# Optimization experiments

Hardware: AMD Instinct MI355X
Metric: run time of the kernel (lower is better)

The kernel has to match this reference:

```python
import jax, jax.numpy as jnp
import numpy as np

DIM = 1024
DIM_HEAD = 64
HEADS = 16
NUM_LATENTS = 64
INNER = DIM_HEAD * HEADS  # 1024


def setup_inputs() -> dict:
    key = jax.random.key(0)
    ks = jax.random.split(key, 6)
    b, m, n = 8, 4, 1024
    x = jax.random.normal(ks[0], (b, m, n, DIM), dtype=jnp.float32)
    latents = jax.random.normal(ks[1], (NUM_LATENTS, DIM), dtype=jnp.float32)
    # Linear weights stored as (in, out); no bias for q/kv, bias for out (matches nn.Linear defaults)
    Wq = jax.random.normal(ks[2], (DIM, INNER), dtype=jnp.float32) * (DIM ** -0.5)
    Wkv = jax.random.normal(ks[3], (DIM, INNER * 2), dtype=jnp.float32) * (DIM ** -0.5)
    Wout = jax.random.normal(ks[4], (INNER, DIM), dtype=jnp.float32) * (INNER ** -0.5)
    bout = jax.random.normal(ks[5], (DIM,), dtype=jnp.float32) * 0.01
    return {"x": x, "latents": latents, "Wq": Wq, "Wkv": Wkv, "Wout": Wout, "bout": bout}


def reference(x, latents, Wq, Wkv, Wout, bout):
    b, m, n, d = x.shape
    h, dh = HEADS, DIM_HEAD
    scale = dh ** -0.5

    # q from latents: [n_lat, inner] -> [h, i, dh]
    q = (latents @ Wq).reshape(NUM_LATENTS, h, dh).transpose(1, 0, 2) * scale

    # k, v from media tokens: [b, m, n, 2*inner] -> two [b, h, m, n, dh]
    kv = x @ Wkv
    k, v = jnp.split(kv, 2, axis=-1)
    k = k.reshape(b, m, n, h, dh).transpose(0, 3, 1, 2, 4)  # b h m n dh
    v = v.reshape(b, m, n, h, dh).transpose(0, 3, 1, 2, 4)

    # latent k, v: [n_lat, 2*inner] -> [h, n_lat, dh] broadcast to [b, h, m, n_lat, dh]
    lkv = latents @ Wkv
    lk, lv = jnp.split(lkv, 2, axis=-1)
    lk = jnp.broadcast_to(lk.reshape(NUM_LATENTS, h, dh).transpose(1, 0, 2)[None, :, None], (b, h, m, NUM_LATENTS, dh))
    lv = jnp.broadcast_to(lv.reshape(NUM_LATENTS, h, dh).transpose(1, 0, 2)[None, :, None], (b, h, m, NUM_LATENTS, dh))

    k = jnp.concatenate((k, lk), axis=-2)  # b h m (n + n_lat) dh
    v = jnp.concatenate((v, lv), axis=-2)

    sim = jnp.einsum('hid,bhmjd->bhmij', q, k)
    attn = jax.nn.softmax(sim, axis=-1)  # stable softmax (max-subtract internal)
    out = jnp.einsum('bhmij,bhmjd->bhmid', attn, v)  # b h m i dh
    out = out.transpose(0, 2, 3, 1, 4).reshape(b, m, NUM_LATENTS, h * dh)  # b m i inner
    return out @ Wout + bout
```

## Files before the change

kernel.cpp:

```cpp
#include <hip/hip_runtime.h>
#include <cstdint>

typedef __attribute__((ext_vector_type(8))) __bf16 bf16x8;
typedef __attribute__((ext_vector_type(4))) float f32x4;
typedef __attribute__((ext_vector_type(8))) unsigned short u16x8;
typedef __attribute__((ext_vector_type(4))) unsigned short u16x4;

__device__ __forceinline__ unsigned short f2bf(float f) {
    union { float f; unsigned u; } v; v.f = f;
    unsigned u = v.u;
    return (unsigned short)((u + 0x7FFFu + ((u >> 16) & 1u)) >> 16);
}

__device__ __forceinline__ void gload_lds16(const void* g, void* l) {
    auto gp = reinterpret_cast<__attribute__((address_space(1))) unsigned*>(
        reinterpret_cast<uintptr_t>(g));
    auto lp = reinterpret_cast<__attribute__((address_space(3))) unsigned*>(
        reinterpret_cast<uintptr_t>(l));
    __builtin_amdgcn_global_load_lds(gp, lp, 16, 0, 0);
}

__global__ __launch_bounds__(256) void cvt_kernel(const float* __restrict__ in,
                                                  unsigned short* __restrict__ out, int n4) {
    int idx = blockIdx.x * 256 + threadIdx.x;
    int stride = gridDim.x * 256;
    for (int i = idx; i < n4; i += stride) {
        float4 v = ((const float4*)in)[i];
        u16x4 o;
        o.x = f2bf(v.x); o.y = f2bf(v.y); o.z = f2bf(v.z); o.w = f2bf(v.w);
        ((u16x4*)out)[i] = o;
    }
}

__global__ __launch_bounds__(256) void transpose_cvt(const float* __restrict__ in,
                                                     unsigned short* __restrict__ out,
                                                     int R, int C) {
    __shared__ float t[32][33];
    int c0 = blockIdx.x * 32, r0 = blockIdx.y * 32;
    int tx = threadIdx.x, ty = threadIdx.y;
    for (int i = ty; i < 32; i += 8)
        t[i][tx] = in[(size_t)(r0 + i) * C + c0 + tx];
    __syncthreads();
    for (int i = ty; i < 32; i += 8)
        out[(size_t)(c0 + i) * R + r0 + tx] = f2bf(t[tx][i]);
}

__global__ __launch_bounds__(256) void gemm128p(const unsigned short* __restrict__ A,
                                                const unsigned short* __restrict__ Bt,
                                                void* __restrict__ C,
                                                const float* __restrict__ bias,
                                                unsigned short* __restrict__ vT,
                                                int M, int N, int K, float scale, int split,
                                                int c_f32, int vstart) {
    __shared__ unsigned short lds[3][2][4096];
    int ntx = N >> 7;
    int nwg = gridDim.x, bid = blockIdx.x, swz = bid;
    if ((nwg & 7) == 0) { int cpx = nwg >> 3; swz = (bid & 7) * cpx + (bid >> 3); }
    int m0 = (swz / ntx) << 7, n0 = (swz % ntx) << 7;
    int tid = threadIdx.x, lane = tid & 63, w = tid >> 6;
    int wm = w >> 1, wn = w & 1;
    int lr = lane & 15, lg = lane >> 4;
    int gq = lg ^ ((lr >> 1) & 3);
    int nkt = K >> 5;

    int arow = tid >> 2;
    int sgl = (tid & 3) ^ ((arow >> 1) & 3);
    int ra0 = m0 + arow;      if (ra0 > M - 1) ra0 = M - 1;
    int ra1 = m0 + 64 + arow; if (ra1 > M - 1) ra1 = M - 1;
    const unsigned short* a0 = A + (size_t)ra0 * K + (sgl << 3);
    const unsigned short* a1 = A + (size_t)ra1 * K + (sgl << 3);
    const unsigned short* b0 = Bt + (size_t)(n0 + arow) * K + (sgl << 3);
    const unsigned short* b1 = Bt + (size_t)(n0 + 64 + arow) * K + (sgl << 3);

    f32x4 acc[4][4] = {};

#define ST_A128(bi, kt) do { \
        gload_lds16(a0 + ((kt) << 5), &lds[bi][0][w << 9]); \
        gload_lds16(a1 + ((kt) << 5), &lds[bi][0][2048 + (w << 9)]); } while (0)
#define ST_B128(bi, kt) do { \
        gload_lds16(b0 + ((kt) << 5), &lds[bi][1][w << 9]); \
        gload_lds16(b1 + ((kt) << 5), &lds[bi][1][2048 + (w << 9)]); } while (0)

    ST_A128(0, 0); ST_B128(0, 0);
    ST_A128(1, 1); ST_B128(1, 1);

    int buf = 0;
    for (int t = 0; t < nkt; ++t) {
        asm volatile("s_waitcnt vmcnt(4) lgkmcnt(0)" ::: "memory");
        __builtin_amdgcn_sched_barrier(0);
        __builtin_amdgcn_s_barrier();
        __builtin_amdgcn_sched_barrier(0);
        int st = t + 2; if (st >= nkt) st = nkt - 1;
        int sbuf = buf + 2; if (sbuf >= 3) sbuf -= 3;
        ST_A128(sbuf, st);
        ST_B128(sbuf, st);
        const unsigned short* pa = &lds[buf][0][((wm << 6) + lr) * 32 + (gq << 3)];
        const unsigned short* pb = &lds[buf][1][((wn << 6) + lr) * 32 + (gq << 3)];
        bf16x8 af[4], bfr[4];
#pragma unroll
        for (int nt = 0; nt < 4; nt++) bfr[nt] = *(const bf16x8*)(pb + nt * 512);
#pragma unroll
        for (int mt = 0; mt < 4; mt++) af[mt] = *(const bf16x8*)(pa + mt * 512);
        __builtin_amdgcn_s_setprio(1);
#pragma unroll
        for (int mt = 0; mt < 4; mt++)
#pragma unroll
            for (int nt = 0; nt < 4; nt++)
                acc[mt][nt] = __builtin_amdgcn_mfma_f32_16x16x32_bf16(af[mt], bfr[nt], acc[mt][nt], 0, 0, 0);
        __builtin_amdgcn_s_setprio(0);
        buf++; if (buf == 3) buf = 0;
    }
#undef ST_A128
#undef ST_B128

#pragma unroll
    for (int mt = 0; mt < 4; mt++) {
#pragma unroll
        for (int nt = 0; nt < 4; nt++) {
            int col = n0 + (wn << 6) + (nt << 4) + lr;
            float sc = (col < split) ? scale : 1.0f;
            float bv = bias ? bias[col] : 0.0f;
#pragma unroll
            for (int r = 0; r < 4; r++) {
                int row = m0 + (wm << 6) + (mt << 4) + (lg << 2) + r;
                if (row < M) {
                    float v = acc[mt][nt][r] * sc + bv;
                    if (vT && col >= vstart) vT[(size_t)(col - vstart) * 64 + row] = f2bf(v);
                    else if (c_f32) ((float*)C)[(size_t)row * N + col] = v;
                    else ((unsigned short*)C)[(size_t)row * N + col] = f2bf(v);
                }
            }
        }
    }
}

__global__ __launch_bounds__(512, 2) void gemm256(const unsigned short* __restrict__ A,
                                                  const unsigned short* __restrict__ Bt,
                                                  unsigned short* __restrict__ kb,
                                                  unsigned short* __restrict__ vbT,
                                                  int M, int N, int K) {
    __shared__ unsigned short lds[2][32768];
    int nkt = K >> 6;
    int ntx = N >> 8;
    int nwg = gridDim.x, bid = blockIdx.x, swz = bid;
    if ((nwg & 7) == 0) { int cpx = nwg >> 3; swz = (bid & 7) * cpx + (bid >> 3); }
    int m0 = (swz / ntx) << 8, n0 = (swz % ntx) << 8;
    int tid = threadIdx.x, lane = tid & 63, w = tid >> 6;
    int wm = w >> 2, wn = w & 3;
    int lr = lane & 15, lg = lane >> 4;

    int srow = lane >> 3;
    int sg = (lane & 7) ^ srow;
    const unsigned short* aS = A + (size_t)(m0 + (w << 3) + srow) * K + (sg << 3);
    const unsigned short* bS = Bt + (size_t)(n0 + (w << 3) + srow) * K + (sg << 3);
    size_t rs64 = (size_t)64 * K;

    int baseA = (wm << 13) + lr * 64;
    int baseB = 16384 + (wn << 12) + lr * 64;
    int kg0 = (((0 << 2) + lg) ^ (lr & 7)) << 3;
    int kg1 = (((1 << 2) + lg) ^ (lr & 7)) << 3;

    f32x4 acc[8][4] = {};

#define ST_A(bi, kt) do { \
        gload_lds16(aS + ((size_t)(kt) << 6),          &lds[bi][(w << 9)]); \
        gload_lds16(aS + rs64 + ((size_t)(kt) << 6),   &lds[bi][4096 + (w << 9)]); \
        gload_lds16(aS + 2*rs64 + ((size_t)(kt) << 6), &lds[bi][8192 + (w << 9)]); \
        gload_lds16(aS + 3*rs64 + ((size_t)(kt) << 6), &lds[bi][12288 + (w << 9)]); } while (0)
#define ST_B(bi, kt) do { \
        gload_lds16(bS + ((size_t)(kt) << 6),          &lds[bi][16384 + (w << 9)]); \
        gload_lds16(bS + rs64 + ((size_t)(kt) << 6),   &lds[bi][20480 + (w << 9)]); \
        gload_lds16(bS + 2*rs64 + ((size_t)(kt) << 6), &lds[bi][24576 + (w << 9)]); \
        gload_lds16(bS + 3*rs64 + ((size_t)(kt) << 6), &lds[bi][28672 + (w << 9)]); } while (0)

    ST_A(0, 0);
    ST_B(0, 0);

    for (int t = 0; t < nkt; ++t) {
        int cur = t & 1, nxt = cur ^ 1;
        int st = t + 1; if (st >= nkt) st = nkt - 1;
        const unsigned short* L = &lds[cur][0];
        bf16x8 af[4], bfr[4];

        ST_A(nxt, st);
        __builtin_amdgcn_sched_barrier(0);
        asm volatile("s_waitcnt vmcnt(4)" ::: "memory");
        __builtin_amdgcn_sched_barrier(0);
        __builtin_amdgcn_s_barrier();
        __builtin_amdgcn_sched_barrier(0);
#pragma unroll
        for (int nt = 0; nt < 4; nt++) bfr[nt] = *(const bf16x8*)(L + baseB + nt * 1024 + kg0);
#pragma unroll
        for (int i = 0; i < 4; i++) af[i] = *(const bf16x8*)(L + baseA + i * 1024 + kg0);
        asm volatile("s_waitcnt lgkmcnt(0)" ::: "memory");
        __builtin_amdgcn_sched_barrier(0);
        __builtin_amdgcn_s_setprio(1);
#pragma unroll
        for (int i = 0; i < 4; i++)
#pragma unroll
            for (int nt = 0; nt < 4; nt++)
                acc[i][nt] = __builtin_amdgcn_mfma_f32_16x16x32_bf16(af[i], bfr[nt], acc[i][nt], 0, 0, 0);
        __builtin_amdgcn_s_setprio(0);

        ST_B(nxt, st);
#pragma unroll
        for (int i = 0; i < 4; i++) af[i] = *(const bf16x8*)(L + baseA + (i + 4) * 1024 + kg0);
        asm volatile("s_waitcnt lgkmcnt(0)" ::: "memory");
        __builtin_amdgcn_sched_barrier(0);
        __builtin_amdgcn_s_setprio(1);
#pragma unroll
        for (int i = 0; i < 4; i++)
#pragma unroll
            for (int nt = 0; nt < 4; nt++)
                acc[i + 4][nt] = __builtin_amdgcn_mfma_f32_16x16x32_bf16(af[i], bfr[nt], acc[i + 4][nt], 0, 0, 0);
        __builtin_amdgcn_s_setprio(0);

#pragma unroll
        for (int nt = 0; nt < 4; nt++) bfr[nt] = *(const bf16x8*)(L + baseB + nt * 1024 + kg1);
#pragma unroll
        for (int i = 0; i < 4; i++) af[i] = *(const bf16x8*)(L + baseA + i * 1024 + kg1);
        asm volatile("s_waitcnt lgkmcnt(0)" ::: "memory");
        __builtin_amdgcn_sched_barrier(0);
        __builtin_amdgcn_s_setprio(1);
#pragma unroll
        for (int i = 0; i < 4; i++)
#pragma unroll
            for (int nt = 0; nt < 4; nt++)
                acc[i][nt] = __builtin_amdgcn_mfma_f32_16x16x32_bf16(af[i], bfr[nt], acc[i][nt], 0, 0, 0);
        __builtin_amdgcn_s_setprio(0);

#pragma unroll
        for (int i = 0; i < 4; i++) af[i] = *(const bf16x8*)(L + baseA + (i + 4) * 1024 + kg1);
        asm volatile("s_waitcnt lgkmcnt(0)" ::: "memory");
        __builtin_amdgcn_sched_barrier(0);
        __builtin_amdgcn_s_barrier();
        __builtin_amdgcn_sched_barrier(0);
        __builtin_amdgcn_s_setprio(1);
#pragma unroll
        for (int i = 0; i < 4; i++)
#pragma unroll
            for (int nt = 0; nt < 4; nt++)
                acc[i + 4][nt] = __builtin_amdgcn_mfma_f32_16x16x32_bf16(af[i], bfr[nt], acc[i + 4][nt], 0, 0, 0);
        __builtin_amdgcn_s_setprio(0);
    }
#undef ST_A
#undef ST_B

    if (n0 < 1024) {
#pragma unroll
        for (int mt = 0; mt < 8; mt++) {
#pragma unroll
            for (int nt = 0; nt < 4; nt++) {
                int col = n0 + (wn << 6) + (nt << 4) + lr;
                size_t rbase = (size_t)(m0 + (wm << 7) + (mt << 4) + (lg << 2));
#pragma unroll
                for (int r = 0; r < 4; r++)
                    kb[(rbase + r) * 1024 + col] = f2bf(acc[mt][nt][r]);
            }
        }
    } else {
#pragma unroll
        for (int mt = 0; mt < 8; mt++) {
#pragma unroll
            for (int nt = 0; nt < 4; nt++) {
                int dg = n0 - 1024 + (wn << 6) + (nt << 4) + lr;
                int rbase = m0 + (wm << 7) + (mt << 4) + (lg << 2);
                int bm = rbase >> 10, j = rbase & 1023;
                u16x4 o;
                o.x = f2bf(acc[mt][nt][0]); o.y = f2bf(acc[mt][nt][1]);
                o.z = f2bf(acc[mt][nt][2]); o.w = f2bf(acc[mt][nt][3]);
                *(u16x4*)(&vbT[((size_t)(bm << 10) + dg) * 1024 + j]) = o;
            }
        }
    }
}

__global__ __launch_bounds__(256) void attn_kernel(const unsigned short* __restrict__ qg, int qstride,
                                                   const unsigned short* __restrict__ kb,
                                                   const unsigned short* __restrict__ vbT,
                                                   const unsigned short* __restrict__ lkg, int lstride,
                                                   const unsigned short* __restrict__ lvT,
                                                   unsigned short* __restrict__ og) {
    __shared__ unsigned short K_lds[64 * 72];
    __shared__ unsigned short V_lds[64 * 72];
    __shared__ unsigned short P_lds[4][16 * 72];
    int bm = blockIdx.x >> 4, h = blockIdx.x & 15;
    int tid = threadIdx.x, lane = tid & 63, w = tid >> 6;
    int lr = lane & 15, lg = lane >> 4;

    bf16x8 qf[2];
#pragma unroll
    for (int kk = 0; kk < 2; kk++)
        qf[kk] = *(const bf16x8*)(qg + (size_t)((w << 4) + lr) * qstride + (h << 6) + (kk << 5) + (lg << 3));

    f32x4 acc[4] = {};
    float m_run[4], l_run[4];
#pragma unroll
    for (int r = 0; r < 4; r++) { m_run[r] = -1e30f; l_run[r] = 0.0f; }

    int jrow = tid >> 2;
    int seg = (tid & 3) << 4;

    const unsigned short* k_s = kb + (size_t)((bm << 10) + jrow) * 1024 + (h << 6) + seg;
    const unsigned short* v_s = vbT + (size_t)((bm << 10) + (h << 6) + jrow) * 1024 + seg;
    u16x8 k0 = *(const u16x8*)(k_s);
    u16x8 k1 = *(const u16x8*)(k_s + 8);
    u16x8 v0 = *(const u16x8*)(v_s);
    u16x8 v1 = *(const u16x8*)(v_s + 8);

    for (int t = 0; t < 17; t++) {
        *(u16x8*)(&K_lds[jrow * 72 + seg]) = k0;
        *(u16x8*)(&K_lds[jrow * 72 + seg + 8]) = k1;
        *(u16x8*)(&V_lds[jrow * 72 + seg]) = v0;
        *(u16x8*)(&V_lds[jrow * 72 + seg + 8]) = v1;
        __syncthreads();

        u16x8 nk0 = k0, nk1 = k1, nv0 = v0, nv1 = v1;
        if (t < 16) {
            if (t < 15) {
                const unsigned short* ks = kb + (size_t)((bm << 10) + ((t + 1) << 6) + jrow) * 1024 + (h << 6) + seg;
                const unsigned short* vs = vbT + (size_t)((bm << 10) + (h << 6) + jrow) * 1024 + ((t + 1) << 6) + seg;
                nk0 = *(const u16x8*)(ks);
                nk1 = *(const u16x8*)(ks + 8);
                nv0 = *(const u16x8*)(vs);
                nv1 = *(const u16x8*)(vs + 8);
            } else {
                const unsigned short* ks = lkg + (size_t)jrow * lstride + (h << 6) + seg;
                const unsigned short* vs = lvT + (size_t)((h << 6) + jrow) * 64 + seg;
                nk0 = *(const u16x8*)(ks);
                nk1 = *(const u16x8*)(ks + 8);
                nv0 = *(const u16x8*)(vs);
                nv1 = *(const u16x8*)(vs + 8);
            }
        }

        f32x4 s[4] = {};
#pragma unroll
        for (int jt = 0; jt < 4; jt++) {
#pragma unroll
            for (int kk = 0; kk < 2; kk++) {
                bf16x8 kf = *(const bf16x8*)(&K_lds[(size_t)((jt << 4) + lr) * 72 + (kk << 5) + (lg << 3)]);
                s[jt] = __builtin_amdgcn_mfma_f32_16x16x32_bf16(qf[kk], kf, s[jt], 0, 0, 0);
            }
        }
#pragma unroll
        for (int r = 0; r < 4; r++) {
            float mx = fmaxf(fmaxf(s[0][r], s[1][r]), fmaxf(s[2][r], s[3][r]));
            mx = fmaxf(mx, __shfl_xor(mx, 1));
            mx = fmaxf(mx, __shfl_xor(mx, 2));
            mx = fmaxf(mx, __shfl_xor(mx, 4));
            mx = fmaxf(mx, __shfl_xor(mx, 8));
            float nm = fmaxf(m_run[r], mx);
            float fct = __expf(m_run[r] - nm);
            m_run[r] = nm;
            float p0 = __expf(s[0][r] - nm);
            float p1 = __expf(s[1][r] - nm);
            float p2 = __expf(s[2][r] - nm);
            float p3 = __expf(s[3][r] - nm);
            float sum = p0 + p1 + p2 + p3;
            sum += __shfl_xor(sum, 1);
            sum += __shfl_xor(sum, 2);
            sum += __shfl_xor(sum, 4);
            sum += __shfl_xor(sum, 8);
            l_run[r] = l_run[r] * fct + sum;
#pragma unroll
            for (int dt = 0; dt < 4; dt++) acc[dt][r] *= fct;
            int prow = ((lg << 2) + r) * 72;
            P_lds[w][prow + lr]      = f2bf(p0);
            P_lds[w][prow + 16 + lr] = f2bf(p1);
            P_lds[w][prow + 32 + lr] = f2bf(p2);
            P_lds[w][prow + 48 + lr] = f2bf(p3);
        }
#pragma unroll
        for (int jkk = 0; jkk < 2; jkk++) {
            bf16x8 pf = *(const bf16x8*)(&P_lds[w][(size_t)lr * 72 + (jkk << 5) + (lg << 3)]);
#pragma unroll
            for (int dt = 0; dt < 4; dt++) {
                bf16x8 vf = *(const bf16x8*)(&V_lds[(size_t)((dt << 4) + lr) * 72 + (jkk << 5) + (lg << 3)]);
                acc[dt] = __builtin_amdgcn_mfma_f32_16x16x32_bf16(pf, vf, acc[dt], 0, 0, 0);
            }
        }
        __syncthreads();
        k0 = nk0; k1 = nk1; v0 = nv0; v1 = nv1;
    }
#pragma unroll
    for (int dt = 0; dt < 4; dt++) {
#pragma unroll
        for (int r = 0; r < 4; r++) {
            int i = (w << 4) + (lg << 2) + r;
            float v = acc[dt][r] / l_run[r];
            og[(size_t)((bm << 6) + i) * 1024 + (h << 6) + (dt << 4) + lr] = f2bf(v);
        }
    }
}

extern "C" void kernel_launch(void* const* d_in, const int* in_sizes, int n_in,
                              void* d_out, int out_size, void* d_ws, size_t ws_size,
                              hipStream_t stream) {
    const float* x       = (const float*)d_in[0];
    const float* latents = (const float*)d_in[1];
    const float* Wq      = (const float*)d_in[2];
    const float* Wkv     = (const float*)d_in[3];
    const float* Wout    = (const float*)d_in[4];
    const float* bout    = (const float*)d_in[5];
    char* ws = (char*)d_ws;
    unsigned short* xb    = (unsigned short*)(ws);
    unsigned short* kb    = (unsigned short*)(ws + 67108864);
    unsigned short* vbT   = (unsigned short*)(ws + 134217728);
    unsigned short* wqkvt = (unsigned short*)(ws + 201326592);
    unsigned short* wkvt  = wqkvt + 1024 * 1024;
    unsigned short* woutt = (unsigned short*)(ws + 207618048);
    unsigned short* latb  = (unsigned short*)(ws + 209715200);
    unsigned short* qlkvb = (unsigned short*)(ws + 209846272);
    unsigned short* attnb = (unsigned short*)(ws + 210239488);
    unsigned short* lvT   = (unsigned short*)(ws + 214433792);

    cvt_kernel<<<2048, 256, 0, stream>>>(x, xb, 33554432 / 4);
    cvt_kernel<<<64, 256, 0, stream>>>(latents, latb, 65536 / 4);
    dim3 tb(32, 8);
    transpose_cvt<<<dim3(32, 32), tb, 0, stream>>>(Wq, wqkvt, 1024, 1024);
    transpose_cvt<<<dim3(64, 32), tb, 0, stream>>>(Wkv, wkvt, 1024, 2048);
    transpose_cvt<<<dim3(32, 32), tb, 0, stream>>>(Wout, woutt, 1024, 1024);
    gemm128p<<<24, 256, 0, stream>>>(latb, wqkvt, qlkvb, nullptr, lvT, 64, 3072, 1024, 0.125f, 1024, 0, 2048);
    gemm256<<<1024, 512, 0, stream>>>(xb, wkvt, kb, vbT, 32768, 2048, 1024);
    attn_kernel<<<512, 256, 0, stream>>>(qlkvb, 3072, kb, vbT, qlkvb + 1024, 3072, lvT, attnb);
    gemm128p<<<128, 256, 0, stream>>>(attnb, woutt, (void*)d_out, bout, nullptr, 2048, 1024, 1024, 1.0f, 0, 1, 1 << 30);
}
```

Before: 257.7 us.

## Fuse conversion kernels into one prep launch and merge latent GEMM into main GEMM

The separate x/latents conversion kernels and the three weight transpose-convert kernels are folded into a single `prep` kernel that dispatches on block index. The small latent QKV GEMM is folded into the large KV GEMM launch as 24 extra leading blocks, so the two GEMMs share one grid and can run side by side. This removes several kernel launches and the serialization gaps between them. In exchange, the latent-GEMM blocks run with 512 threads where the body expects 256: both halves repeat the same loads and write identical results, which wastes some bandwidth.

```diff
diff --git a/kernel.cpp b/kernel.cpp
--- a/kernel.cpp
+++ b/kernel.cpp
@@ -20,24 +20,44 @@
     __builtin_amdgcn_global_load_lds(gp, lp, 16, 0, 0);
 }
 
-__global__ __launch_bounds__(256) void cvt_kernel(const float* __restrict__ in,
-                                                  unsigned short* __restrict__ out, int n4) {
-    int idx = blockIdx.x * 256 + threadIdx.x;
-    int stride = gridDim.x * 256;
-    for (int i = idx; i < n4; i += stride) {
-        float4 v = ((const float4*)in)[i];
+__global__ __launch_bounds__(256) void prep(const float* __restrict__ x,
+                                            const float* __restrict__ latents,
+                                            const float* __restrict__ Wq,
+                                            const float* __restrict__ Wkv,
+                                            const float* __restrict__ Wout,
+                                            unsigned short* __restrict__ xb,
+                                            unsigned short* __restrict__ latb,
+                                            unsigned short* __restrict__ wqkvt,
+                                            unsigned short* __restrict__ wkvt,
+                                            unsigned short* __restrict__ woutt) {
+    int b = blockIdx.x, tid = threadIdx.x;
+    if (b < 2048) {
+        int idx = b * 256 + tid, stride = 2048 * 256;
+        for (int i = idx; i < 8388608; i += stride) {
+            float4 v = ((const float4*)x)[i];
+            u16x4 o;
+            o.x = f2bf(v.x); o.y = f2bf(v.y); o.z = f2bf(v.z); o.w = f2bf(v.w);
+            ((u16x4*)xb)[i] = o;
+        }
+        return;
+    }
+    b -= 2048;
+    if (b < 64) {
+        int i = b * 256 + tid;
+        float4 v = ((const float4*)latents)[i];
         u16x4 o;
         o.x = f2bf(v.x); o.y = f2bf(v.y); o.z = f2bf(v.z); o.w = f2bf(v.w);
-        ((u16x4*)out)[i] = o;
-    }
-}
-
-__global__ __launch_bounds__(256) void transpose_cvt(const float* __restrict__ in,
-                                                     unsigned short* __restrict__ out,
-                                                     int R, int C) {
+        ((u16x4*)latb)[i] = o;
+        return;
+    }
+    b -= 64;
+    const float* in; unsigned short* out; int R, C, bx, by;
+    if (b < 1024)      { in = Wq;   out = wqkvt; R = 1024; C = 1024; bx = b & 31; by = b >> 5; }
+    else if (b < 3072) { int v = b - 1024; in = Wkv;  out = wkvt;  R = 1024; C = 2048; bx = v & 63; by = v >> 6; }
+    else               { int v = b - 3072; in = Wout; out = woutt; R = 1024; C = 1024; bx = v & 31; by = v >> 5; }
     __shared__ float t[32][33];
-    int c0 = blockIdx.x * 32, r0 = blockIdx.y * 32;
-    int tx = threadIdx.x, ty = threadIdx.y;
+    int c0 = bx * 32, r0 = by * 32;
+    int tx = tid & 31, ty = tid >> 5;
     for (int i = ty; i < 32; i += 8)
         t[i][tx] = in[(size_t)(r0 + i) * C + c0 + tx];
     __syncthreads();
@@ -45,19 +65,21 @@
         out[(size_t)(c0 + i) * R + r0 + tx] = f2bf(t[tx][i]);
 }
 
-__global__ __launch_bounds__(256) void gemm128p(const unsigned short* __restrict__ A,
-                                                const unsigned short* __restrict__ Bt,
-                                                void* __restrict__ C,
-                                                const float* __restrict__ bias,
-                                                unsigned short* __restrict__ vT,
-                                                int M, int N, int K, float scale, int split,
-                                                int c_f32, int vstart) {
-    __shared__ unsigned short lds[3][2][4096];
+__device__ __forceinline__ void gemm128p_body(const unsigned short* __restrict__ A,
+                                              const unsigned short* __restrict__ Bt,
+                                              void* __restrict__ C,
+                                              const float* __restrict__ bias,
+                                              unsigned short* __restrict__ vT,
+                                              int M, int N, int K, float scale, int split,
+                                              int c_f32, int vstart,
+                                              int tid, int bid, int nwg,
+                                              unsigned short* ldsbuf) {
+#define LDSP(bi, half) (ldsbuf + ((bi) * 2 + (half)) * 4096)
     int ntx = N >> 7;
-    int nwg = gridDim.x, bid = blockIdx.x, swz = bid;
+    int swz = bid;
     if ((nwg & 7) == 0) { int cpx = nwg >> 3; swz = (bid & 7) * cpx + (bid >> 3); }
     int m0 = (swz / ntx) << 7, n0 = (swz % ntx) << 7;
-    int tid = threadIdx.x, lane = tid & 63, w = tid >> 6;
+    int lane = tid & 63, w = tid >> 6;
     int wm = w >> 1, wn = w & 1;
     int lr = lane & 15, lg = lane >> 4;
     int gq = lg ^ ((lr >> 1) & 3);
@@ -75,11 +97,11 @@
     f32x4 acc[4][4] = {};
 
 #define ST_A128(bi, kt) do { \
-        gload_lds16(a0 + ((kt) << 5), &lds[bi][0][w << 9]); \
-        gload_lds16(a1 + ((kt) << 5), &lds[bi][0][2048 + (w << 9)]); } while (0)
+        gload_lds16(a0 + ((kt) << 5), LDSP(bi, 0) + (w << 9)); \
+        gload_lds16(a1 + ((kt) << 5), LDSP(bi, 0) + 2048 + (w << 9)); } while (0)
 #define ST_B128(bi, kt) do { \
-        gload_lds16(b0 + ((kt) << 5), &lds[bi][1][w << 9]); \
-        gload_lds16(b1 + ((kt) << 5), &lds[bi][1][2048 + (w << 9)]); } while (0)
+        gload_lds16(b0 + ((kt) << 5), LDSP(bi, 1) + (w << 9)); \
+        gload_lds16(b1 + ((kt) << 5), LDSP(bi, 1) + 2048 + (w << 9)); } while (0)
 
     ST_A128(0, 0); ST_B128(0, 0);
     ST_A128(1, 1); ST_B128(1, 1);
@@ -94,8 +116,8 @@
         int sbuf = buf + 2; if (sbuf >= 3) sbuf -= 3;
         ST_A128(sbuf, st);
         ST_B128(sbuf, st);
-        const unsigned short* pa = &lds[buf][0][((wm << 6) + lr) * 32 + (gq << 3)];
-        const unsigned short* pb = &lds[buf][1][((wn << 6) + lr) * 32 + (gq << 3)];
+        const unsigned short* pa = LDSP(buf, 0) + ((wm << 6) + lr) * 32 + (gq << 3);
+        const unsigned short* pb = LDSP(buf, 1) + ((wn << 6) + lr) * 32 + (gq << 3);
         bf16x8 af[4], bfr[4];
 #pragma unroll
         for (int nt = 0; nt < 4; nt++) bfr[nt] = *(const bf16x8*)(pb + nt * 512);
@@ -112,6 +134,7 @@
     }
 #undef ST_A128
 #undef ST_B128
+#undef LDSP
 
 #pragma unroll
     for (int mt = 0; mt < 4; mt++) {
@@ -134,15 +157,39 @@
     }
 }
 
-__global__ __launch_bounds__(512, 2) void gemm256(const unsigned short* __restrict__ A,
-                                                  const unsigned short* __restrict__ Bt,
-                                                  unsigned short* __restrict__ kb,
-                                                  unsigned short* __restrict__ vbT,
-                                                  int M, int N, int K) {
+__global__ __launch_bounds__(256) void gemm128p(const unsigned short* __restrict__ A,
+                                                const unsigned short* __restrict__ Bt,
+                                                void* __restrict__ C,
+                                                const float* __restrict__ bias,
+                                                unsigned short* __restrict__ vT,
+                                                int M, int N, int K, float scale, int split,
+                                                int c_f32, int vstart) {
+    __shared__ unsigned short lds[3 * 2 * 4096];
+    gemm128p_body(A, Bt, C, bias, vT, M, N, K, scale, split, c_f32, vstart,
+                  threadIdx.x, blockIdx.x, gridDim.x, lds);
+}
+
+__global__ __launch_bounds__(512, 2) void mega(const unsigned short* __restrict__ latb,
+                                               const unsigned short* __restrict__ wqkvt,
+                                               unsigned short* __restrict__ qlkvb,
+                                               unsigned short* __restrict__ lvT,
+                                               const unsigned short* __restrict__ A,
+                                               const unsigned short* __restrict__ Bt,
+                                               unsigned short* __restrict__ kb,
+                                               unsigned short* __restrict__ vbT,
+                                               int M, int N, int K) {
     __shared__ unsigned short lds[2][32768];
+
+    if (blockIdx.x < 24) {
+        gemm128p_body(latb, wqkvt, qlkvb, nullptr, lvT, 64, 3072, 1024, 0.125f, 1024, 0, 2048,
+                      threadIdx.x & 255, blockIdx.x, 24, &lds[0][0]);
+        return;
+    }
+
     int nkt = K >> 6;
     int ntx = N >> 8;
-    int nwg = gridDim.x, bid = blockIdx.x, swz = bid;
+    int nwg = (M >> 8) * (N >> 8);
+    int bid = blockIdx.x - 24, swz = bid;
     if ((nwg & 7) == 0) { int cpx = nwg >> 3; swz = (bid & 7) * cpx + (bid >> 3); }
     int m0 = (swz / ntx) << 8, n0 = (swz % ntx) << 8;
     int tid = threadIdx.x, lane = tid & 63, w = tid >> 6;
@@ -415,14 +462,8 @@
     unsigned short* attnb = (unsigned short*)(ws + 210239488);
     unsigned short* lvT   = (unsigned short*)(ws + 214433792);
 
-    cvt_kernel<<<2048, 256, 0, stream>>>(x, xb, 33554432 / 4);
-    cvt_kernel<<<64, 256, 0, stream>>>(latents, latb, 65536 / 4);
-    dim3 tb(32, 8);
-    transpose_cvt<<<dim3(32, 32), tb, 0, stream>>>(Wq, wqkvt, 1024, 1024);
-    transpose_cvt<<<dim3(64, 32), tb, 0, stream>>>(Wkv, wkvt, 1024, 2048);
-    transpose_cvt<<<dim3(32, 32), tb, 0, stream>>>(Wout, woutt, 1024, 1024);
-    gemm128p<<<24, 256, 0, stream>>>(latb, wqkvt, qlkvb, nullptr, lvT, 64, 3072, 1024, 0.125f, 1024, 0, 2048);
-    gemm256<<<1024, 512, 0, stream>>>(xb, wkvt, kb, vbT, 32768, 2048, 1024);
+    prep<<<6208, 256, 0, stream>>>(x, latents, Wq, Wkv, Wout, xb, latb, wqkvt, wkvt, woutt);
+    mega<<<1048, 512, 0, stream>>>(latb, wqkvt, qlkvb, lvT, xb, wkvt, kb, vbT, 32768, 2048, 1024);
     attn_kernel<<<512, 256, 0, stream>>>(qlkvb, 3072, kb, vbT, qlkvb + 1024, 3072, lvT, attnb);
     gemm128p<<<128, 256, 0, stream>>>(attnb, woutt, (void*)d_out, bout, nullptr, 2048, 1024, 1024, 1.0f, 0, 1, 1 << 30);
 }
```

Result: faster. 241.9 us (-6.1%).
